# Performance work log

Measured on AMD Instinct MI355X. Metric: run time of the kernel, lower is better.

The kernel has to match this reference:

```python
import jax, jax.numpy as jnp
import numpy as np
import math

B, M, DM = 8, 512, 1024
H, DH = 16, 64
R_ATTN, R_WO, R_FF, DFF = 32, 512, 256, 4096
EPS = 1e-12  # BERT LayerNorm eps


def _layernorm(x, w, b):
    mu = jnp.mean(x, axis=-1, keepdims=True)
    var = jnp.mean(jnp.square(x - mu), axis=-1, keepdims=True)
    return (x - mu) * jax.lax.rsqrt(var + EPS) * w + b


def setup_inputs() -> dict:
    key = jax.random.key(0)
    ks = jax.random.split(key, 24)
    s = 0.02
    return {
        "x": jax.random.normal(ks[0], (B, M, DM), jnp.float32),
        "mask": jnp.zeros((B, M), jnp.float32),  # additive mask, 0 = attend
        "Pq": jax.random.normal(ks[1], (H, DM, R_ATTN), jnp.float32) * s,
        "Vq": jax.random.normal(ks[2], (H, R_ATTN, DH), jnp.float32) * s,
        "bq": jax.random.normal(ks[3], (H, DH), jnp.float32) * s,
        "Pk": jax.random.normal(ks[4], (H, DM, R_ATTN), jnp.float32) * s,
        "Vk": jax.random.normal(ks[5], (H, R_ATTN, DH), jnp.float32) * s,
        "bk": jax.random.normal(ks[6], (H, DH), jnp.float32) * s,
        "Pv": jax.random.normal(ks[7], (H, DM, R_ATTN), jnp.float32) * s,
        "Vv": jax.random.normal(ks[8], (H, R_ATTN, DH), jnp.float32) * s,
        "bv": jax.random.normal(ks[9], (H, DH), jnp.float32) * s,
        "Uo": jax.random.normal(ks[10], (DM, R_WO), jnp.float32) * s,
        "Vo": jax.random.normal(ks[11], (R_WO, DM), jnp.float32) * s,
        "bo_attn": jax.random.normal(ks[12], (DM,), jnp.float32) * s,
        "U1": jax.random.normal(ks[13], (DM, R_FF), jnp.float32) * s,
        "V1": jax.random.normal(ks[14], (R_FF, DFF), jnp.float32) * s,
        "b1": jax.random.normal(ks[15], (DFF,), jnp.float32) * s,
        "U2": jax.random.normal(ks[16], (DFF, R_FF), jnp.float32) * s,
        "V2": jax.random.normal(ks[17], (R_FF, DM), jnp.float32) * s,
        "b2": jax.random.normal(ks[18], (DM,), jnp.float32) * s,
        "ln1_w": jnp.ones((DM,), jnp.float32),
        "ln1_b": jnp.zeros((DM,), jnp.float32),
        "ln2_w": jnp.ones((DM,), jnp.float32),
        "ln2_b": jnp.zeros((DM,), jnp.float32),
    }


def reference(x, mask, Pq, Vq, bq, Pk, Vk, bk, Pv, Vv, bv,
              Uo, Vo, bo_attn, U1, V1, b1, U2, V2, b2,
              ln1_w, ln1_b, ln2_w, ln2_b):
    Bx, Mx, dm = x.shape
    dh = Vq.shape[-1]
    scale = 1.0 / math.sqrt(dh)

    def proj(P, V, b):
        # low-rank factorized per-head projection: (x @ P_h) @ V_h + b_h
        low = jnp.einsum('bmd,hdr->bhmr', x, P)      # [B,H,M,R]
        return jnp.einsum('bhmr,hrd->bhmd', low, V) + b[None, :, None, :]

    q = proj(Pq, Vq, bq)
    k = proj(Pk, Vk, bk)
    v = proj(Pv, Vv, bv)

    scores = jnp.einsum('bhmd,bhnd->bhmn', q, k) * scale
    scores = scores + mask[:, None, None, :]        # additive mask over keys
    attn = jax.nn.softmax(scores, axis=-1)
    out = jnp.einsum('bhmn,bhnd->bhmd', attn, v)    # [B,H,M,dh]
    attn_out = out.transpose(0, 2, 1, 3).reshape(Bx, Mx, dm)

    x1 = _layernorm(x + (attn_out @ Uo) @ Vo + bo_attn, ln1_w, ln1_b)

    # low-rank FFN: gelu((x1 @ U1) @ V1 + b1) @ U2 @ V2 + b2
    h = jax.nn.gelu((x1 @ U1) @ V1 + b1, approximate=False)
    y = (h @ U2) @ V2 + b2
    return _layernorm(x1 + y, ln2_w, ln2_b)
```

## Files before the change

kernel.cpp:

```cpp
#include <hip/hip_runtime.h>
#include <hip/hip_bf16.h>

typedef short short8 __attribute__((ext_vector_type(8)));
typedef float f32x4 __attribute__((ext_vector_type(4)));

#define DEV static __device__ __forceinline__

DEV unsigned short f2bu(float f) {
  __hip_bfloat16 h = __float2bfloat16(f);
  unsigned short u;
  __builtin_memcpy(&u, &h, 2);
  return u;
}
DEV float bu2f(unsigned short u) {
  union { unsigned int i; float f; } x;
  x.i = ((unsigned int)u) << 16;
  return x.f;
}

DEV float gelu_f(float v) {
  float e = __expf(-1.702f * v);
  return v * __builtin_amdgcn_rcpf(1.0f + e);
}

typedef const __attribute__((address_space(1))) unsigned int gu32;
typedef __attribute__((address_space(3))) unsigned int lu32;
DEV void gload16(const void* g, void* l) {
  __builtin_amdgcn_global_load_lds((gu32*)g, (lu32*)l, 16, 0, 0);
}

#define VMW(n) asm volatile("s_waitcnt vmcnt(" #n ")" ::: "memory")
#define LG0()  asm volatile("s_waitcnt lgkmcnt(0)" ::: "memory")
DEV void barm() {
  asm volatile("" ::: "memory");
  __builtin_amdgcn_s_barrier();
  asm volatile("" ::: "memory");
}


__global__ __launch_bounds__(256) void convx_kernel(const float* __restrict__ src,
                                                    unsigned short* __restrict__ dst, int n4) {
  int i = blockIdx.x * 256 + threadIdx.x;
  if (i >= n4) return;
  float4 v = reinterpret_cast<const float4*>(src)[i];
  ushort4 o;
  o.x = f2bu(v.x); o.y = f2bu(v.y); o.z = f2bu(v.z); o.w = f2bu(v.w);
  reinterpret_cast<ushort4*>(dst)[i] = o;
}

struct TJob {
  const float* s;
  unsigned short* d;
  long ss, ds;
  int R, C, cpt, tpb;
  int nt, pad;
};
struct TJobs { TJob j[12]; };

__global__ __launch_bounds__(256) void tconvall_kernel(TJobs js) {
  __shared__ float t[32][33];
  int idx = blockIdx.x, e = 0;
  while (idx >= js.j[e].nt) { idx -= js.j[e].nt; e++; }
  const TJob J = js.j[e];
  int bat = idx / J.tpb;
  int tt = idx - bat * J.tpb;
  int rt = tt / J.cpt, ct = tt - rt * J.cpt;
  const float* s = J.s + (size_t)bat * J.ss;
  unsigned short* d = J.d + (size_t)bat * J.ds;
  int r0 = rt * 32, c0 = ct * 32;
  int tr = threadIdx.x >> 5, tc = threadIdx.x & 31;
#pragma unroll
  for (int i = 0; i < 4; i++)
    t[tr + i * 8][tc] = s[(size_t)(r0 + tr + i * 8) * J.C + c0 + tc];
  __syncthreads();
#pragma unroll
  for (int i = 0; i < 4; i++)
    d[(size_t)(c0 + tr + i * 8) * J.R + r0 + tc] = f2bu(t[tc][tr + i * 8]);
}

#define EPI_BF16 0
#define EPI_F32  1
#define EPI_GELU 2

template <int EPI>
__global__ __launch_bounds__(256) void gemm_kernel(const unsigned short* __restrict__ A,
                                                   const unsigned short* __restrict__ Bt,
                                                   void* __restrict__ C,
                                                   const float* __restrict__ bias,
                                                   int M, int N, int K) {
  __shared__ unsigned short As0[128 * 64];
  __shared__ unsigned short Bs0[128 * 64];
  __shared__ unsigned short As1[128 * 64];
  __shared__ unsigned short Bs1[128 * 64];
  const int tid = threadIdx.x;
  const int l = tid & 63, w = tid >> 6;
  const int wm = w >> 1, wn = w & 1;
  const int lm = l & 15, lg = l >> 4;

  int nwg = gridDim.x * gridDim.y;
  int bid = blockIdx.x + gridDim.x * blockIdx.y;
  int nb = ((nwg & 7) == 0) ? ((bid & 7) * (nwg >> 3) + (bid >> 3)) : bid;
  int bm = nb % gridDim.x, bn = nb / gridDim.x;
  const int m0 = bm * 128, n0 = bn * 128;

  int klen = K, k0 = 0;
  float* Cf = (float*)C;
  if (gridDim.z > 1) {
    klen = K / gridDim.z;
    k0 = blockIdx.z * klen;
    Cf += (size_t)blockIdx.z * (size_t)M * (size_t)N;
  }

  f32x4 acc[4][4];
#pragma unroll
  for (int fi = 0; fi < 4; fi++)
#pragma unroll
    for (int fj = 0; fj < 4; fj++) acc[fi][fj] = (f32x4){0.f, 0.f, 0.f, 0.f};

  auto stage = [&](unsigned short* As, unsigned short* Bs, int kt) {
    const unsigned short* Ab = A + (size_t)m0 * K + k0 + kt;
    const unsigned short* Bb = Bt + (size_t)n0 * K + k0 + kt;
#pragma unroll
    for (int i = 0; i < 4; i++) {
      int c = ((w * 4 + i) << 6) + l;
      int r = c >> 3, pch = c & 7;
      int so = ((pch ^ (r & 7)) << 3);
      gload16(Ab + (size_t)r * K + so, &As[(w * 4 + i) << 9]);
      gload16(Bb + (size_t)r * K + so, &Bs[(w * 4 + i) << 9]);
    }
  };

  auto compute = [&](const unsigned short* As, const unsigned short* Bs) {
#pragma unroll
    for (int ks = 0; ks < 2; ks++) {
      short8 af[4], bfr[4];
#pragma unroll
      for (int f = 0; f < 4; f++) {
        int ra = wm * 64 + f * 16 + lm;
        af[f] = *reinterpret_cast<const short8*>(&As[(ra << 6) + (((ks * 4 + lg) ^ (ra & 7)) << 3)]);
        int rb = wn * 64 + f * 16 + lm;
        bfr[f] = *reinterpret_cast<const short8*>(&Bs[(rb << 6) + (((ks * 4 + lg) ^ (rb & 7)) << 3)]);
      }
#pragma unroll
      for (int fi = 0; fi < 4; fi++)
#pragma unroll
        for (int fj = 0; fj < 4; fj++)
          acc[fi][fj] = __builtin_amdgcn_mfma_f32_16x16x32_bf16(af[fi], bfr[fj], acc[fi][fj], 0, 0, 0);
    }
  };

  stage(As0, Bs0, 0);
  stage(As1, Bs1, 64);

  int kt = 0;
  for (; kt < klen - 128; kt += 128) {
    VMW(8); barm();
    compute(As0, Bs0);
    LG0(); barm();
    stage(As0, Bs0, kt + 128);
    VMW(8); barm();
    compute(As1, Bs1);
    LG0(); barm();
    stage(As1, Bs1, kt + 192);
  }
  VMW(8); barm();
  compute(As0, Bs0);
  VMW(0); barm();
  compute(As1, Bs1);

  float bcol[4];
  if (EPI == EPI_GELU) {
#pragma unroll
    for (int fj = 0; fj < 4; fj++) bcol[fj] = bias[n0 + wn * 64 + fj * 16 + lm];
  }

#pragma unroll
  for (int fi = 0; fi < 4; fi++) {
    int row = m0 + wm * 64 + fi * 16 + (lg << 2);
#pragma unroll
    for (int fj = 0; fj < 4; fj++) {
      int col = n0 + wn * 64 + fj * 16 + lm;
#pragma unroll
      for (int r = 0; r < 4; r++) {
        float v = acc[fi][fj][r];
        size_t off = (size_t)(row + r) * N + col;
        if (EPI == EPI_F32) {
          Cf[off] = v;
        } else if (EPI == EPI_BF16) {
          ((unsigned short*)C)[off] = f2bu(v);
        } else {
          ((unsigned short*)C)[off] = f2bu(gelu_f(v + bcol[fj]));
        }
      }
    }
  }
}

__global__ __launch_bounds__(256) void qkv_kernel(const unsigned short* __restrict__ low,
                                                  const unsigned short* __restrict__ VqT,
                                                  const unsigned short* __restrict__ VkT,
                                                  const unsigned short* __restrict__ VvT,
                                                  const float* __restrict__ bq, const float* __restrict__ bk,
                                                  const float* __restrict__ bv,
                                                  unsigned short* __restrict__ qo,
                                                  unsigned short* __restrict__ ko,
                                                  unsigned short* __restrict__ vo) {
  const int mc = blockIdx.x, h = blockIdx.y, b = blockIdx.z;
  const int tid = threadIdx.x, l = tid & 63, w = tid >> 6;
  const int lm = l & 15, lg = l >> 4;
  const int bh = b * 16 + h;
  const int m0 = mc * 128 + w * 32;

#pragma unroll
  for (int p = 0; p < 3; p++) {
    const unsigned short* VT = (p == 0 ? VqT : (p == 1 ? VkT : VvT));
    const float* bias = (p == 0 ? bq : (p == 1 ? bk : bv));
    unsigned short* out = (p == 0 ? qo : (p == 1 ? ko : vo));
    short8 af[2];
#pragma unroll
    for (int fi = 0; fi < 2; fi++)
      af[fi] = *reinterpret_cast<const short8*>(
          low + (size_t)(b * 512 + m0 + fi * 16 + lm) * 1536 + p * 512 + h * 32 + lg * 8);
#pragma unroll
    for (int nt = 0; nt < 4; nt++) {
      short8 bf = *reinterpret_cast<const short8*>(VT + h * 2048 + (nt * 16 + lm) * 32 + lg * 8);
      float bb = bias[h * 64 + nt * 16 + lm];
#pragma unroll
      for (int fi = 0; fi < 2; fi++) {
        f32x4 acc = (f32x4){0.f, 0.f, 0.f, 0.f};
        acc = __builtin_amdgcn_mfma_f32_16x16x32_bf16(af[fi], bf, acc, 0, 0, 0);
#pragma unroll
        for (int j = 0; j < 4; j++) {
          int row = m0 + fi * 16 + (lg << 2) + j;
          out[((size_t)bh * 512 + row) * 64 + nt * 16 + lm] = f2bu(acc[j] + bb);
        }
      }
    }
  }
}

__global__ __launch_bounds__(256) void vtrans_kernel(const unsigned short* __restrict__ v,
                                                     unsigned short* __restrict__ vt) {
  int i = blockIdx.x * 256 + threadIdx.x;
  int m8i = i & 63, d = (i >> 6) & 63, bh = i >> 12;
  const unsigned short* vb = v + (size_t)bh * 32768;
  short8 o;
#pragma unroll
  for (int j = 0; j < 8; j++) o[j] = (short)vb[(size_t)(m8i * 8 + j) * 64 + d];
  *reinterpret_cast<short8*>(vt + (size_t)bh * 32768 + (size_t)d * 512 + m8i * 8) = o;
}

__global__ __launch_bounds__(256) void attn_kernel(const unsigned short* __restrict__ q,
                                                   const unsigned short* __restrict__ k,
                                                   const unsigned short* __restrict__ vt,
                                                   const float* __restrict__ mask,
                                                   unsigned short* __restrict__ attn_out) {
  __shared__ unsigned short Ks[128 * 64];
  __shared__ unsigned short Vs[64 * 128];
  __shared__ unsigned short Ps[4][32 * 128];

  int bid = blockIdx.x;
  int wid = (bid & 7) * 64 + (bid >> 3);
  const int qt = wid & 3, h = (wid >> 2) & 15, b = wid >> 6;
  const int tid = threadIdx.x, l = tid & 63, w = tid >> 6;
  const int lm = l & 15, lg = l >> 4;
  const int bh = b * 16 + h;
  const int qrow0 = qt * 128 + w * 32;

  const unsigned short* qp = q + ((size_t)bh * 512 + qrow0) * 64;
  short8 aq[2][2];
#pragma unroll
  for (int fi = 0; fi < 2; fi++)
#pragma unroll
    for (int kf = 0; kf < 2; kf++)
      aq[fi][kf] = *reinterpret_cast<const short8*>(qp + (fi * 16 + lm) * 64 + kf * 32 + (lg << 3));

  const unsigned short* kb = k + (size_t)bh * 512 * 64;
  const unsigned short* vb = vt + (size_t)bh * 64 * 512;
  const float* mk = mask + b * 512;

  short8 onesf;
#pragma unroll
  for (int j = 0; j < 8; j++) onesf[j] = (short)0x3F80;

  f32x4 oa[2][5];
#pragma unroll
  for (int fi = 0; fi < 2; fi++)
#pragma unroll
    for (int nd = 0; nd < 5; nd++) oa[fi][nd] = (f32x4){0.f, 0.f, 0.f, 0.f};

  for (int t = 0; t < 4; t++) {
    const int kbase = t * 128;
    __syncthreads();
#pragma unroll
    for (int i = 0; i < 4; i++) {
      int c = ((w * 4 + i) << 6) + l;
      int r = c >> 3, pch = c & 7;
      gload16(kb + (size_t)(kbase + r) * 64 + ((pch ^ (r & 7)) << 3), &Ks[(w * 4 + i) << 9]);
    }
#pragma unroll
    for (int i = 0; i < 4; i++) {
      int c = ((w * 4 + i) << 6) + l;
      int r = c >> 4, pch = c & 15;
      gload16(vb + (size_t)r * 512 + kbase + ((pch ^ (r & 7)) << 3), &Vs[(w * 4 + i) << 9]);
    }
    __syncthreads();

#pragma unroll
    for (int nf = 0; nf < 8; nf++) {
      int krow = nf * 16 + lm;
      int swz = krow & 7;
      short8 b0 = *reinterpret_cast<const short8*>(&Ks[(krow << 6) + ((lg ^ swz) << 3)]);
      short8 b1 = *reinterpret_cast<const short8*>(&Ks[(krow << 6) + (((4 + lg) ^ swz) << 3)]);
      float mv = mk[kbase + krow];
#pragma unroll
      for (int fi = 0; fi < 2; fi++) {
        f32x4 t0 = (f32x4){0.f, 0.f, 0.f, 0.f};
        t0 = __builtin_amdgcn_mfma_f32_16x16x32_bf16(aq[fi][0], b0, t0, 0, 0, 0);
        t0 = __builtin_amdgcn_mfma_f32_16x16x32_bf16(aq[fi][1], b1, t0, 0, 0, 0);
#pragma unroll
        for (int r = 0; r < 4; r++) {
          float e = __expf(t0[r] * 0.125f + mv);
          int prow = fi * 16 + (lg << 2) + r;
          int col = nf * 16 + lm;
          int ch = col >> 3;
          Ps[w][(prow << 7) + (((ch ^ (prow & 7)) << 3) + (col & 7))] = f2bu(e);
        }
      }
    }

#pragma unroll
    for (int kfi = 0; kfi < 4; kfi++) {
      short8 pa[2];
#pragma unroll
      for (int fi = 0; fi < 2; fi++) {
        int prow = fi * 16 + lm;
        pa[fi] = *reinterpret_cast<const short8*>(
            &Ps[w][(prow << 7) + ((((kfi << 2) + lg) ^ (prow & 7)) << 3)]);
      }
#pragma unroll
      for (int nd = 0; nd < 5; nd++) {
        short8 bv;
        if (nd < 4) {
          int vrow = nd * 16 + lm;
          bv = *reinterpret_cast<const short8*>(
              &Vs[(vrow << 7) + ((((kfi << 2) + lg) ^ (vrow & 7)) << 3)]);
        } else {
          bv = onesf;
        }
#pragma unroll
        for (int fi = 0; fi < 2; fi++)
          oa[fi][nd] = __builtin_amdgcn_mfma_f32_16x16x32_bf16(pa[fi], bv, oa[fi][nd], 0, 0, 0);
      }
    }
  }

#pragma unroll
  for (int fi = 0; fi < 2; fi++)
#pragma unroll
    for (int r = 0; r < 4; r++) {
      float inv = 1.0f / oa[fi][4][r];
      int row = qrow0 + fi * 16 + (lg << 2) + r;
#pragma unroll
      for (int nd = 0; nd < 4; nd++)
        attn_out[((size_t)b * 512 + row) * 1024 + h * 64 + nd * 16 + lm] = f2bu(oa[fi][nd][r] * inv);
    }
}

template <bool WB>
__global__ __launch_bounds__(256) void ln_kernel(const float* __restrict__ a,
                                                 const float* badd,
                                                 const float* __restrict__ bias,
                                                 const float* __restrict__ w, const float* __restrict__ bb,
                                                 float* outf, unsigned short* __restrict__ outb) {
  const int t = blockIdx.x, tid = threadIdx.x;
  float4 av = reinterpret_cast<const float4*>(a + (size_t)t * 1024)[tid];
  float4 dv = reinterpret_cast<const float4*>(badd + (size_t)t * 1024)[tid];
  float4 bi = reinterpret_cast<const float4*>(bias)[tid];
  float v0 = av.x + dv.x + bi.x;
  float v1 = av.y + dv.y + bi.y;
  float v2 = av.z + dv.z + bi.z;
  float v3 = av.w + dv.w + bi.w;
  float s = v0 + v1 + v2 + v3;
#pragma unroll
  for (int off = 32; off >= 1; off >>= 1) s += __shfl_xor(s, off);
  __shared__ float red[4], red2[4];
  if ((tid & 63) == 0) red[tid >> 6] = s;
  __syncthreads();
  float mu = (red[0] + red[1] + red[2] + red[3]) * (1.0f / 1024.0f);
  float d0 = v0 - mu, d1 = v1 - mu, d2 = v2 - mu, d3 = v3 - mu;
  float qv = d0 * d0 + d1 * d1 + d2 * d2 + d3 * d3;
#pragma unroll
  for (int off = 32; off >= 1; off >>= 1) qv += __shfl_xor(qv, off);
  if ((tid & 63) == 0) red2[tid >> 6] = qv;
  __syncthreads();
  float var = (red2[0] + red2[1] + red2[2] + red2[3]) * (1.0f / 1024.0f);
  float rs = rsqrtf(var + 1e-12f);
  float4 wv = reinterpret_cast<const float4*>(w)[tid];
  float4 bv = reinterpret_cast<const float4*>(bb)[tid];
  float4 o;
  o.x = d0 * rs * wv.x + bv.x;
  o.y = d1 * rs * wv.y + bv.y;
  o.z = d2 * rs * wv.z + bv.z;
  o.w = d3 * rs * wv.w + bv.w;
  reinterpret_cast<float4*>(outf + (size_t)t * 1024)[tid] = o;
  if (WB) {
    ushort4 ob;
    ob.x = f2bu(o.x); ob.y = f2bu(o.y); ob.z = f2bu(o.z); ob.w = f2bu(o.w);
    reinterpret_cast<ushort4*>(outb + (size_t)t * 1024)[tid] = ob;
  }
}

template <int NP>
__global__ __launch_bounds__(256) void addcvt_kernel(const float* __restrict__ p,
                                                     unsigned short* __restrict__ o, int n4) {
  int i = blockIdx.x * 256 + threadIdx.x;
  if (i >= n4) return;
  float4 a = reinterpret_cast<const float4*>(p)[i];
#pragma unroll
  for (int j = 1; j < NP; j++) {
    float4 bx = reinterpret_cast<const float4*>(p + (size_t)j * n4 * 4)[i];
    a.x += bx.x; a.y += bx.y; a.z += bx.z; a.w += bx.w;
  }
  ushort4 ob;
  ob.x = f2bu(a.x); ob.y = f2bu(a.y); ob.z = f2bu(a.z); ob.w = f2bu(a.w);
  reinterpret_cast<ushort4*>(o)[i] = ob;
}

extern "C" void kernel_launch(void* const* d_in, const int* in_sizes, int n_in,
                              void* d_out, int out_size, void* d_ws, size_t ws_size,
                              hipStream_t stream) {
  const float* x    = (const float*)d_in[0];
  const float* mask = (const float*)d_in[1];
  const float* Pq   = (const float*)d_in[2];
  const float* Vq   = (const float*)d_in[3];
  const float* bq   = (const float*)d_in[4];
  const float* Pk   = (const float*)d_in[5];
  const float* Vk   = (const float*)d_in[6];
  const float* bk   = (const float*)d_in[7];
  const float* Pv   = (const float*)d_in[8];
  const float* Vv   = (const float*)d_in[9];
  const float* bv   = (const float*)d_in[10];
  const float* Uo   = (const float*)d_in[11];
  const float* Vo   = (const float*)d_in[12];
  const float* bo   = (const float*)d_in[13];
  const float* U1   = (const float*)d_in[14];
  const float* V1   = (const float*)d_in[15];
  const float* b1   = (const float*)d_in[16];
  const float* U2   = (const float*)d_in[17];
  const float* V2   = (const float*)d_in[18];
  const float* b2   = (const float*)d_in[19];
  const float* ln1w = (const float*)d_in[20];
  const float* ln1b = (const float*)d_in[21];
  const float* ln2w = (const float*)d_in[22];
  const float* ln2b = (const float*)d_in[23];

  char* ws = (char*)d_ws;
  unsigned short* PcatT = (unsigned short*)(ws + 0);
  unsigned short* UoT   = (unsigned short*)(ws + 3145728);
  unsigned short* VoT   = (unsigned short*)(ws + 4194304);
  unsigned short* U1T   = (unsigned short*)(ws + 5242880);
  unsigned short* V1T   = (unsigned short*)(ws + 5767168);
  unsigned short* U2T   = (unsigned short*)(ws + 7864320);
  unsigned short* V2T   = (unsigned short*)(ws + 9961472);
  unsigned short* xb    = (unsigned short*)(ws + 10485760);
  unsigned short* aob   = (unsigned short*)(ws + 10485760);
  unsigned short* lowb  = (unsigned short*)(ws + 18874368);
  unsigned short* t1b   = (unsigned short*)(ws + 18874368);
  unsigned short* t2b   = (unsigned short*)(ws + 20971520);
  unsigned short* qb    = (unsigned short*)(ws + 31457280);
  unsigned short* kbuf  = (unsigned short*)(ws + 39845888);
  float*          res1  = (float*)(ws + 31457280);
  unsigned short* vbuf  = (unsigned short*)(ws + 48234496);
  unsigned short* vtb   = (unsigned short*)(ws + 56623104);
  float*          skp   = (float*)(ws + 48234496);
  unsigned short* t_ob  = (unsigned short*)(ws + 65011712);
  unsigned short* x1b   = (unsigned short*)(ws + 69206016);
  unsigned short* hb    = (unsigned short*)(ws + 77594624);
  unsigned short* VqT   = (unsigned short*)(ws + 77594624);
  unsigned short* VkT   = (unsigned short*)(ws + 77660160);
  unsigned short* VvT   = (unsigned short*)(ws + 77725696);
  float*          yb    = (float*)d_out;

  convx_kernel<<<4096, 256, 0, stream>>>(x, xb, 1048576);
  TJobs js;
  js.j[0]  = {Pq, PcatT + 0,       32768, 32768, 1024, 32, 1, 32, 512, 0};
  js.j[1]  = {Pk, PcatT + 524288,  32768, 32768, 1024, 32, 1, 32, 512, 0};
  js.j[2]  = {Pv, PcatT + 1048576, 32768, 32768, 1024, 32, 1, 32, 512, 0};
  js.j[3]  = {Uo, UoT, 0, 0, 1024, 512, 16, 512, 512, 0};
  js.j[4]  = {Vo, VoT, 0, 0, 512, 1024, 32, 512, 512, 0};
  js.j[5]  = {U1, U1T, 0, 0, 1024, 256, 8, 256, 256, 0};
  js.j[6]  = {V1, V1T, 0, 0, 256, 4096, 128, 1024, 1024, 0};
  js.j[7]  = {U2, U2T, 0, 0, 4096, 256, 8, 1024, 1024, 0};
  js.j[8]  = {V2, V2T, 0, 0, 256, 1024, 32, 256, 256, 0};
  js.j[9]  = {Vq, VqT, 2048, 2048, 32, 64, 2, 2, 32, 0};
  js.j[10] = {Vk, VkT, 2048, 2048, 32, 64, 2, 2, 32, 0};
  js.j[11] = {Vv, VvT, 2048, 2048, 32, 64, 2, 2, 32, 0};
  tconvall_kernel<<<5216, 256, 0, stream>>>(js);

  gemm_kernel<EPI_BF16><<<dim3(32, 12), 256, 0, stream>>>(xb, PcatT, lowb, nullptr, 4096, 1536, 1024);

  qkv_kernel<<<dim3(4, 16, 8), 256, 0, stream>>>(lowb, VqT, VkT, VvT, bq, bk, bv, qb, kbuf, vbuf);
  vtrans_kernel<<<2048, 256, 0, stream>>>(vbuf, vtb);

  attn_kernel<<<512, 256, 0, stream>>>(qb, kbuf, vtb, mask, aob);

  gemm_kernel<EPI_F32><<<dim3(32, 4, 2), 256, 0, stream>>>(aob, UoT, skp, nullptr, 4096, 512, 1024);
  addcvt_kernel<2><<<2048, 256, 0, stream>>>(skp, t_ob, 524288);
  gemm_kernel<EPI_F32><<<dim3(32, 8), 256, 0, stream>>>(t_ob, VoT, res1, nullptr, 4096, 1024, 512);

  ln_kernel<true><<<4096, 256, 0, stream>>>(x, res1, bo, ln1w, ln1b, res1, x1b);

  gemm_kernel<EPI_F32><<<dim3(32, 2, 2), 256, 0, stream>>>(x1b, U1T, skp, nullptr, 4096, 256, 1024);
  addcvt_kernel<2><<<1024, 256, 0, stream>>>(skp, t1b, 262144);
  gemm_kernel<EPI_GELU><<<dim3(32, 32), 256, 0, stream>>>(t1b, V1T, hb, b1, 4096, 4096, 256);
  gemm_kernel<EPI_F32><<<dim3(32, 2, 2), 256, 0, stream>>>(hb, U2T, skp, nullptr, 4096, 256, 4096);
  addcvt_kernel<2><<<1024, 256, 0, stream>>>(skp, t2b, 262144);
  gemm_kernel<EPI_F32><<<dim3(32, 8), 256, 0, stream>>>(t2b, V2T, yb, nullptr, 4096, 1024, 256);

  ln_kernel<false><<<4096, 256, 0, stream>>>(res1, yb, b2, ln2w, ln2b, yb, nullptr);

  (void)in_sizes; (void)n_in; (void)out_size; (void)ws_size;
}
```

Measured before the change: 202.9 us.

## Store GEMM partials and residual outputs in bf16, raise split-K to four

Split-K partial sums and the Vo/V2 GEMM outputs are now written in bf16 instead of fp32. The reduction kernel reads eight bf16 values per thread, and the LayerNorm kernels read the bf16 residual. The U1 and U2 GEMMs move from split-K 2 to split-K 4 to give more workgroups, the epilogue loop is reordered by row, and the workspace layout is reshuffled. This halves memory traffic for intermediates but adds bf16 rounding on partial sums and pre-LayerNorm values, which risks accuracy.

```diff
diff --git a/kernel.cpp b/kernel.cpp
--- a/kernel.cpp
+++ b/kernel.cpp
@@ -104,12 +104,14 @@
   const int m0 = bm * 128, n0 = bn * 128;
 
   int klen = K, k0 = 0;
-  float* Cf = (float*)C;
+  size_t zoff = 0;
   if (gridDim.z > 1) {
     klen = K / gridDim.z;
     k0 = blockIdx.z * klen;
-    Cf += (size_t)blockIdx.z * (size_t)M * (size_t)N;
-  }
+    zoff = (size_t)blockIdx.z * (size_t)M * (size_t)N;
+  }
+  float* Cf = (float*)C + zoff;
+  unsigned short* Cb = (unsigned short*)C + zoff;
 
   f32x4 acc[4][4];
 #pragma unroll
@@ -178,18 +180,18 @@
   for (int fi = 0; fi < 4; fi++) {
     int row = m0 + wm * 64 + fi * 16 + (lg << 2);
 #pragma unroll
-    for (int fj = 0; fj < 4; fj++) {
-      int col = n0 + wn * 64 + fj * 16 + lm;
-#pragma unroll
-      for (int r = 0; r < 4; r++) {
+    for (int r = 0; r < 4; r++) {
+      size_t rbase = (size_t)(row + r) * N;
+#pragma unroll
+      for (int fj = 0; fj < 4; fj++) {
+        int col = n0 + wn * 64 + fj * 16 + lm;
         float v = acc[fi][fj][r];
-        size_t off = (size_t)(row + r) * N + col;
         if (EPI == EPI_F32) {
-          Cf[off] = v;
+          Cf[rbase + col] = v;
         } else if (EPI == EPI_BF16) {
-          ((unsigned short*)C)[off] = f2bu(v);
+          Cb[rbase + col] = f2bu(v);
         } else {
-          ((unsigned short*)C)[off] = f2bu(gelu_f(v + bcol[fj]));
+          Cb[rbase + col] = f2bu(gelu_f(v + bcol[fj]));
         }
       }
     }
@@ -367,15 +369,21 @@
     }
 }
 
-template <bool WB>
+template <bool WB, bool BB16>
 __global__ __launch_bounds__(256) void ln_kernel(const float* __restrict__ a,
-                                                 const float* badd,
+                                                 const void* __restrict__ badd,
                                                  const float* __restrict__ bias,
                                                  const float* __restrict__ w, const float* __restrict__ bb,
                                                  float* outf, unsigned short* __restrict__ outb) {
   const int t = blockIdx.x, tid = threadIdx.x;
   float4 av = reinterpret_cast<const float4*>(a + (size_t)t * 1024)[tid];
-  float4 dv = reinterpret_cast<const float4*>(badd + (size_t)t * 1024)[tid];
+  float4 dv;
+  if (BB16) {
+    ushort4 u = reinterpret_cast<const ushort4*>((const unsigned short*)badd + (size_t)t * 1024)[tid];
+    dv.x = bu2f(u.x); dv.y = bu2f(u.y); dv.z = bu2f(u.z); dv.w = bu2f(u.w);
+  } else {
+    dv = reinterpret_cast<const float4*>((const float*)badd + (size_t)t * 1024)[tid];
+  }
   float4 bi = reinterpret_cast<const float4*>(bias)[tid];
   float v0 = av.x + dv.x + bi.x;
   float v1 = av.y + dv.y + bi.y;
@@ -412,19 +420,24 @@
 }
 
 template <int NP>
-__global__ __launch_bounds__(256) void addcvt_kernel(const float* __restrict__ p,
-                                                     unsigned short* __restrict__ o, int n4) {
+__global__ __launch_bounds__(256) void addcvt16_kernel(const unsigned short* __restrict__ p,
+                                                       unsigned short* __restrict__ o, int n8) {
   int i = blockIdx.x * 256 + threadIdx.x;
-  if (i >= n4) return;
-  float4 a = reinterpret_cast<const float4*>(p)[i];
+  if (i >= n8) return;
+  float s[8];
+  short8 a = *reinterpret_cast<const short8*>(p + (size_t)i * 8);
+#pragma unroll
+  for (int e = 0; e < 8; e++) s[e] = bu2f((unsigned short)a[e]);
 #pragma unroll
   for (int j = 1; j < NP; j++) {
-    float4 bx = reinterpret_cast<const float4*>(p + (size_t)j * n4 * 4)[i];
-    a.x += bx.x; a.y += bx.y; a.z += bx.z; a.w += bx.w;
-  }
-  ushort4 ob;
-  ob.x = f2bu(a.x); ob.y = f2bu(a.y); ob.z = f2bu(a.z); ob.w = f2bu(a.w);
-  reinterpret_cast<ushort4*>(o)[i] = ob;
+    short8 bx = *reinterpret_cast<const short8*>(p + (size_t)j * n8 * 8 + (size_t)i * 8);
+#pragma unroll
+    for (int e = 0; e < 8; e++) s[e] += bu2f((unsigned short)bx[e]);
+  }
+  short8 ob;
+#pragma unroll
+  for (int e = 0; e < 8; e++) ob[e] = (short)f2bu(s[e]);
+  *reinterpret_cast<short8*>(o + (size_t)i * 8) = ob;
 }
 
 extern "C" void kernel_launch(void* const* d_in, const int* in_sizes, int n_in,
@@ -456,31 +469,35 @@
   const float* ln2b = (const float*)d_in[23];
 
   char* ws = (char*)d_ws;
-  unsigned short* PcatT = (unsigned short*)(ws + 0);
-  unsigned short* UoT   = (unsigned short*)(ws + 3145728);
-  unsigned short* VoT   = (unsigned short*)(ws + 4194304);
-  unsigned short* U1T   = (unsigned short*)(ws + 5242880);
-  unsigned short* V1T   = (unsigned short*)(ws + 5767168);
-  unsigned short* U2T   = (unsigned short*)(ws + 7864320);
-  unsigned short* V2T   = (unsigned short*)(ws + 9961472);
-  unsigned short* xb    = (unsigned short*)(ws + 10485760);
-  unsigned short* aob   = (unsigned short*)(ws + 10485760);
-  unsigned short* lowb  = (unsigned short*)(ws + 18874368);
-  unsigned short* t1b   = (unsigned short*)(ws + 18874368);
-  unsigned short* t2b   = (unsigned short*)(ws + 20971520);
-  unsigned short* qb    = (unsigned short*)(ws + 31457280);
-  unsigned short* kbuf  = (unsigned short*)(ws + 39845888);
-  float*          res1  = (float*)(ws + 31457280);
-  unsigned short* vbuf  = (unsigned short*)(ws + 48234496);
-  unsigned short* vtb   = (unsigned short*)(ws + 56623104);
-  float*          skp   = (float*)(ws + 48234496);
-  unsigned short* t_ob  = (unsigned short*)(ws + 65011712);
-  unsigned short* x1b   = (unsigned short*)(ws + 69206016);
-  unsigned short* hb    = (unsigned short*)(ws + 77594624);
-  unsigned short* VqT   = (unsigned short*)(ws + 77594624);
-  unsigned short* VkT   = (unsigned short*)(ws + 77660160);
-  unsigned short* VvT   = (unsigned short*)(ws + 77725696);
-  float*          yb    = (float*)d_out;
+  unsigned short* PcatT  = (unsigned short*)(ws + 0);
+  unsigned short* UoT    = (unsigned short*)(ws + 3145728);
+  unsigned short* VoT    = (unsigned short*)(ws + 4194304);
+  unsigned short* U1T    = (unsigned short*)(ws + 5242880);
+  unsigned short* V1T    = (unsigned short*)(ws + 5767168);
+  unsigned short* U2T    = (unsigned short*)(ws + 7864320);
+  unsigned short* V2T    = (unsigned short*)(ws + 9961472);
+  unsigned short* xb     = (unsigned short*)(ws + 10485760);
+  unsigned short* aob    = (unsigned short*)(ws + 10485760);
+  unsigned short* lowb   = (unsigned short*)(ws + 18874368);
+  unsigned short* t1b    = (unsigned short*)(ws + 18874368);
+  unsigned short* t2b    = (unsigned short*)(ws + 20971520);
+  unsigned short* qb     = (unsigned short*)(ws + 31457280);
+  unsigned short* kbuf   = (unsigned short*)(ws + 39845888);
+  unsigned short* vbuf   = (unsigned short*)(ws + 48234496);
+  unsigned short* vtb    = (unsigned short*)(ws + 56623104);
+  unsigned short* res1b  = (unsigned short*)(ws + 31457280);
+  float*          res1f  = (float*)(ws + 39845888);
+  unsigned short* skpo   = (unsigned short*)(ws + 56623104);
+  unsigned short* t_ob   = (unsigned short*)(ws + 65011712);
+  unsigned short* x1b    = (unsigned short*)(ws + 69206016);
+  unsigned short* skp2   = (unsigned short*)(ws + 65011712);
+  unsigned short* yb16   = (unsigned short*)(ws + 65011712);
+  unsigned short* hb     = (unsigned short*)(ws + 77594624);
+  unsigned short* skp1   = (unsigned short*)(ws + 77594624);
+  unsigned short* VqT    = (unsigned short*)(ws + 110100480);
+  unsigned short* VkT    = (unsigned short*)(ws + 110166016);
+  unsigned short* VvT    = (unsigned short*)(ws + 110231552);
+  float*          yb     = (float*)d_out;
 
   convx_kernel<<<4096, 256, 0, stream>>>(x, xb, 1048576);
   TJobs js;
@@ -505,20 +522,20 @@
 
   attn_kernel<<<512, 256, 0, stream>>>(qb, kbuf, vtb, mask, aob);
 
-  gemm_kernel<EPI_F32><<<dim3(32, 4, 2), 256, 0, stream>>>(aob, UoT, skp, nullptr, 4096, 512, 1024);
-  addcvt_kernel<2><<<2048, 256, 0, stream>>>(skp, t_ob, 524288);
-  gemm_kernel<EPI_F32><<<dim3(32, 8), 256, 0, stream>>>(t_ob, VoT, res1, nullptr, 4096, 1024, 512);
-
-  ln_kernel<true><<<4096, 256, 0, stream>>>(x, res1, bo, ln1w, ln1b, res1, x1b);
-
-  gemm_kernel<EPI_F32><<<dim3(32, 2, 2), 256, 0, stream>>>(x1b, U1T, skp, nullptr, 4096, 256, 1024);
-  addcvt_kernel<2><<<1024, 256, 0, stream>>>(skp, t1b, 262144);
+  gemm_kernel<EPI_BF16><<<dim3(32, 4, 2), 256, 0, stream>>>(aob, UoT, skpo, nullptr, 4096, 512, 1024);
+  addcvt16_kernel<2><<<1024, 256, 0, stream>>>(skpo, t_ob, 262144);
+  gemm_kernel<EPI_BF16><<<dim3(32, 8), 256, 0, stream>>>(t_ob, VoT, res1b, nullptr, 4096, 1024, 512);
+
+  ln_kernel<true, true><<<4096, 256, 0, stream>>>(x, res1b, bo, ln1w, ln1b, res1f, x1b);
+
+  gemm_kernel<EPI_BF16><<<dim3(32, 2, 4), 256, 0, stream>>>(x1b, U1T, skp1, nullptr, 4096, 256, 1024);
+  addcvt16_kernel<4><<<512, 256, 0, stream>>>(skp1, t1b, 131072);
   gemm_kernel<EPI_GELU><<<dim3(32, 32), 256, 0, stream>>>(t1b, V1T, hb, b1, 4096, 4096, 256);
-  gemm_kernel<EPI_F32><<<dim3(32, 2, 2), 256, 0, stream>>>(hb, U2T, skp, nullptr, 4096, 256, 4096);
-  addcvt_kernel<2><<<1024, 256, 0, stream>>>(skp, t2b, 262144);
-  gemm_kernel<EPI_F32><<<dim3(32, 8), 256, 0, stream>>>(t2b, V2T, yb, nullptr, 4096, 1024, 256);
-
-  ln_kernel<false><<<4096, 256, 0, stream>>>(res1, yb, b2, ln2w, ln2b, yb, nullptr);
+  gemm_kernel<EPI_BF16><<<dim3(32, 2, 4), 256, 0, stream>>>(hb, U2T, skp2, nullptr, 4096, 256, 4096);
+  addcvt16_kernel<4><<<512, 256, 0, stream>>>(skp2, t2b, 131072);
+  gemm_kernel<EPI_BF16><<<dim3(32, 8), 256, 0, stream>>>(t2b, V2T, yb16, nullptr, 4096, 1024, 256);
+
+  ln_kernel<false, true><<<4096, 256, 0, stream>>>(res1f, yb16, b2, ln2w, ln2b, yb, nullptr);
 
   (void)in_sizes; (void)n_in; (void)out_size; (void)ws_size;
 }
```

Result: faster. 187.4 us (-7.6%).
